# Performance work log

Hardware: AMD Instinct MI355X
Metric: run time of the kernel (lower is better)

The kernel has to match this reference:

```python
import jax, jax.numpy as jnp
import numpy as np

B, C, H, W = 32, 128, 56, 56
O = 256
KH, KW = 3, 3
SH, SW = 1, 1
PH, PW = 1, 1
T = 6          # num_terms
R = 8          # low_rank
D = C * KH * KW          # 1152
R2 = R * KH * KW         # 72


def setup_inputs() -> dict:
    key = jax.random.key(0)
    ks = jax.random.split(key, 6)
    scale = 0.05
    return {
        "x": jax.random.normal(ks[0], (B, C, H, W), dtype=jnp.float32),
        "S1s": jax.random.normal(ks[1], (T, D, R), dtype=jnp.float32) * scale,
        "U1s": jax.random.normal(ks[2], (T, R, O), dtype=jnp.float32) * scale,
        "U2s": jax.random.normal(ks[3], (T, R2, D), dtype=jnp.float32) * scale,
        "S2s": jax.random.normal(ks[4], (T, R2, O), dtype=jnp.float32) * scale,
        "bias": jax.random.normal(ks[5], (O,), dtype=jnp.float32) * scale,
    }


def _extract_windows(x):
    # im2col: pad then gather strided windows; d flattened in (C, kh, kw) order
    xp = jnp.pad(x, ((0, 0), (0, 0), (PH, PH), (PW, PW)))
    Hp, Wp = xp.shape[2], xp.shape[3]
    Ho = (Hp - KH) // SH + 1
    Wo = (Wp - KW) // SW + 1
    # stack KH*KW shifted views -> [B, C, KH*KW, Ho, Wo]
    patches = jnp.stack(
        [xp[:, :, i:i + SH * Ho:SH, j:j + SW * Wo:SW]
         for i in range(KH) for j in range(KW)],
        axis=2,
    )
    # -> [B, Ho, Wo, C, KH*KW] -> [N, C*KH*KW]
    xw = patches.transpose(0, 3, 4, 1, 2).reshape(B * Ho * Wo, D)
    return xw, Ho, Wo


def reference(x, S1s, U1s, U2s, S2s, bias):
    xw, Ho, Wo = _extract_windows(x)                    # [N, D]
    # term 1: x_windows @ S1s[t] @ U1s[t], averaged over terms
    out1 = jnp.einsum('nd,tdr,tro->no', xw, S1s, U1s, optimize=True) / T + bias
    # term 2: x_windows @ U2s[t].T @ S2s[t], averaged over terms
    out2 = jnp.einsum('nd,tdr,tro->no', xw, jnp.swapaxes(U2s, 1, 2), S2s,
                      optimize=True) / T
    # NOTE: bias is added twice, faithfully matching the original module
    out = (out1 + out2 + bias).reshape(B, Ho, Wo, O).transpose(0, 3, 1, 2)
    return out
```

## Files before the change

kernel.cpp:

```cpp
#include <hip/hip_runtime.h>
#include <hip/hip_bf16.h>

typedef __attribute__((ext_vector_type(8))) short  short8;
typedef __attribute__((ext_vector_type(8))) unsigned short ushort8;
typedef __attribute__((ext_vector_type(4))) unsigned short usv4;
typedef __attribute__((ext_vector_type(4))) float  f32x4;

#define D_DIM 1152
#define O_DIM 256
#define N_TOT 100352
#define XT_H 58
#define XT_ROW (58 * 128)

__device__ __forceinline__ unsigned short f2bf(float f) {
  __hip_bfloat16 h = __float2bfloat16(f);
  return __builtin_bit_cast(unsigned short, h);
}

#define GLOAD_LDS16(g, l)                                              \
  __builtin_amdgcn_global_load_lds(                                    \
      (const __attribute__((address_space(1))) void*)(g),              \
      (__attribute__((address_space(3))) void*)(l), 16, 0, 0)

__global__ __launch_bounds__(256) void wt_kernel(
    const float* __restrict__ S1s, const float* __restrict__ U1s,
    const float* __restrict__ U2s, const float* __restrict__ S2s,
    unsigned short* __restrict__ Wt) {
  __shared__ float A_lds[32][64];
  __shared__ float B_lds[32][64];

  const int bo = blockIdx.x & 3;
  const int bd = blockIdx.x >> 2;
  const int o0  = bo << 6;
  const int dn0 = bd << 6;
  const int rr  = dn0 >> 7;
  const int c0  = dn0 & 127;

  const int tid = threadIdx.x;
  const int ty = tid >> 4, tx = tid & 15;

  float acc[4][4] = {};

  for (int kc = 0; kc < 15; ++kc) {
#pragma unroll
    for (int e = 0; e < 8; ++e) {
      const int li = e * 256 + tid;
      const int kk = li >> 6;
      const int xx = li & 63;
      const int k  = kc * 32 + kk;
      float av, bv;
      if (k < 48) {
        av = U1s[k * O_DIM + o0 + xx];
        const int d_old = (c0 + xx) * 9 + rr;
        bv = S1s[(size_t)((k >> 3) * D_DIM + d_old) * 8 + (k & 7)];
      } else {
        const int kq = k - 48;
        av = S2s[(size_t)kq * O_DIM + o0 + xx];
        const int d_old = (c0 + xx) * 9 + rr;
        bv = U2s[(size_t)kq * D_DIM + d_old];
      }
      A_lds[kk][xx] = av;
      B_lds[kk][xx] = bv;
    }
    __syncthreads();
#pragma unroll
    for (int kk = 0; kk < 32; ++kk) {
      f32x4 a = *(const f32x4*)&A_lds[kk][ty << 2];
      f32x4 b = *(const f32x4*)&B_lds[kk][tx << 2];
#pragma unroll
      for (int i = 0; i < 4; ++i)
#pragma unroll
        for (int j = 0; j < 4; ++j)
          acc[i][j] += a[i] * b[j];
    }
    __syncthreads();
  }

#pragma unroll
  for (int i = 0; i < 4; ++i) {
    usv4 v;
#pragma unroll
    for (int j = 0; j < 4; ++j) v[j] = f2bf(acc[i][j] * (1.0f / 6.0f));
    *(usv4*)(Wt + (size_t)(o0 + (ty << 2) + i) * D_DIM + dn0 + (tx << 2)) = v;
  }
}

__global__ __launch_bounds__(256) void pad_kernel(const float* __restrict__ x,
                                                  unsigned short* __restrict__ xt) {
  int blk = blockIdx.x;
  int b = blk / XT_H, ih = blk - b * XT_H;
  unsigned short* dst = xt + (size_t)blk * XT_ROW;
  int tid = threadIdx.x;

  if (ih == 0 || ih == XT_H - 1) {
    ushort8 z;
#pragma unroll
    for (int q = 0; q < 8; ++q) z[q] = 0;
    for (int i = tid; i < XT_ROW / 8; i += 256) ((ushort8*)dst)[i] = z;
    return;
  }

  __shared__ unsigned short lds[128 * 58];
  int h = ih - 1;
  const float* xb = x + (size_t)b * 128 * 3136 + (size_t)h * 56;
#pragma unroll 4
  for (int r = 0; r < 28; ++r) {
    int idx = r * 256 + tid;
    int c = idx / 56, w2 = idx - c * 56;
    lds[c * 58 + w2] = f2bf(xb[(size_t)c * 3136 + w2]);
  }
  __syncthreads();
#pragma unroll 4
  for (int r = 0; r < 29; ++r) {
    int idx = r * 256 + tid;
    int iw = idx >> 7, c = idx & 127;
    unsigned short v = 0;
    if (iw >= 1 && iw <= 56) v = lds[c * 58 + (iw - 1)];
    dst[idx] = v;
  }
}

__device__ __forceinline__ constexpr int KOF(int kt) {
  int rr = kt >> 1;
  return ((rr / 3) * 58 + (rr % 3)) * 128 + (kt & 1) * 64;
}

#define STAGE_S(s_) do {                                                       \
  GLOAD_LDS16(pA0 + (s_) * 32, smem + ((s_) & 3) * 16384 + (tid << 3));        \
  GLOAD_LDS16(pA1 + (s_) * 32, smem + ((s_) & 3) * 16384 + 4096 + (tid << 3)); \
  GLOAD_LDS16(pB0 + KOF((s_) >> 1) + ((s_) & 1) * 32,                          \
              smem + ((s_) & 3) * 16384 + 8192 + (tid << 3));                  \
  GLOAD_LDS16(pB1 + KOF((s_) >> 1) + ((s_) & 1) * 32,                          \
              smem + ((s_) & 3) * 16384 + 12288 + (tid << 3));                 \
} while (0)

#define AFRAG(q_, row_)                                                        \
  (*(const short8*)((const char*)smem + (q_) * 32768 + (row_) * 64 +          \
      ((((lane >> 4) ^ (((row_) >> 1) & 3)) << 4))))
#define BFRAG(q_, row_)                                                        \
  (*(const short8*)((const char*)smem + (q_) * 32768 + 16384 + (row_) * 64 +  \
      ((((lane >> 4) ^ (((row_) >> 1) & 3)) << 4))))

__global__ __launch_bounds__(512, 1) void gemm_kernel(
    const unsigned short* __restrict__ Wt, const unsigned short* __restrict__ xt,
    const float* __restrict__ bias, float* __restrict__ out) {
  __shared__ __align__(1024) unsigned short smem[65536];

  const int bid   = blockIdx.x;
  const int ntile = (bid & 7) * 49 + (bid >> 3);
  const int n0    = ntile << 8;

  const int tid  = threadIdx.x;
  const int lane = tid & 63;
  const int w    = tid >> 6;
  const int wm   = w >> 2;
  const int wn   = w & 3;
  const int la15 = lane & 15;

  const int srow = tid >> 2;
  const int glog = (tid & 3) ^ ((tid >> 3) & 3);
  const unsigned short* pA0 = Wt + (size_t)srow * D_DIM + glog * 8;
  const unsigned short* pA1 = Wt + (size_t)(128 + srow) * D_DIM + glog * 8;
  const unsigned short *pB0, *pB1;
  {
    int n_g = n0 + srow;
    int b = n_g / 3136, s = n_g - b * 3136;
    int oh = s / 56, ow = s - oh * 56;
    pB0 = xt + (((size_t)b * XT_H + oh) * XT_H + ow) * 128 + glog * 8;
    n_g = n0 + 128 + srow;
    b = n_g / 3136; s = n_g - b * 3136;
    oh = s / 56; ow = s - oh * 56;
    pB1 = xt + (((size_t)b * XT_H + oh) * XT_H + ow) * 128 + glog * 8;
  }

  f32x4 acc[8][4] = {};

  STAGE_S(0);
  STAGE_S(1);
  STAGE_S(2);
  asm volatile("s_waitcnt vmcnt(8)" ::: "memory");
  __builtin_amdgcn_s_barrier();

#pragma unroll
  for (int s = 0; s < 36; ++s) {
    const int q = s & 3;

    short8 afr[8], bfr[4];
#pragma unroll
    for (int mi = 0; mi < 8; ++mi)
      afr[mi] = AFRAG(q, (wm << 7) + (mi << 4) + la15);
#pragma unroll
    for (int ni = 0; ni < 4; ++ni)
      bfr[ni] = BFRAG(q, (wn << 6) + (ni << 4) + la15);

    if (s + 3 < 36) STAGE_S(s + 3);

    if (s <= 32)      asm volatile("s_waitcnt vmcnt(8) lgkmcnt(0)" ::: "memory");
    else if (s == 33) asm volatile("s_waitcnt vmcnt(4) lgkmcnt(0)" ::: "memory");
    else              asm volatile("s_waitcnt vmcnt(0) lgkmcnt(0)" ::: "memory");
    if (s < 35) __builtin_amdgcn_s_barrier();
    __builtin_amdgcn_sched_barrier(0);

    __builtin_amdgcn_s_setprio(1);
#pragma unroll
    for (int mi = 0; mi < 8; ++mi)
#pragma unroll
      for (int ni = 0; ni < 4; ++ni)
        acc[mi][ni] = __builtin_amdgcn_mfma_f32_16x16x32_bf16(
            afr[mi], bfr[ni], acc[mi][ni], 0, 0, 0);
    __builtin_amdgcn_s_setprio(0);
  }

  const int lr = (lane >> 4) << 2;
#pragma unroll
  for (int ni = 0; ni < 4; ++ni) {
    const int ng = n0 + (wn << 6) + (ni << 4) + la15;
    const int b  = ng / 3136;
    const int s  = ng - b * 3136;
    float* op = out + (size_t)b * (O_DIM * 3136) + s;
#pragma unroll
    for (int mi = 0; mi < 8; ++mi) {
      const int og = (wm << 7) + (mi << 4) + lr;
#pragma unroll
      for (int r = 0; r < 4; ++r)
        op[(size_t)(og + r) * 3136] = acc[mi][ni][r] + 2.0f * bias[og + r];
    }
  }
}

extern "C" void kernel_launch(void* const* d_in, const int* in_sizes, int n_in,
                              void* d_out, int out_size, void* d_ws, size_t ws_size,
                              hipStream_t stream) {
  const float* x    = (const float*)d_in[0];
  const float* S1s  = (const float*)d_in[1];
  const float* U1s  = (const float*)d_in[2];
  const float* U2s  = (const float*)d_in[3];
  const float* S2s  = (const float*)d_in[4];
  const float* bias = (const float*)d_in[5];
  float* out = (float*)d_out;
  (void)ws_size;

  unsigned short* xt = (unsigned short*)d_ws;
  unsigned short* Wt = (unsigned short*)((char*)d_ws + (size_t)32 * XT_H * XT_ROW * 2);

  pad_kernel<<<dim3(32 * XT_H), dim3(256), 0, stream>>>(x, xt);
  wt_kernel<<<dim3(72), dim3(256), 0, stream>>>(S1s, U1s, U2s, S2s, Wt);
  gemm_kernel<<<dim3(392), dim3(512), 0, stream>>>(Wt, xt, bias, out);
}
```

Baseline: 122.2 us.

## Shrink GEMM tile to 256x128 with 3-stage LDS ring for two blocks per CU

```diff
diff --git a/kernel.cpp b/kernel.cpp
--- a/kernel.cpp
+++ b/kernel.cpp
@@ -120,86 +120,80 @@
   }
 }
 
-__device__ __forceinline__ constexpr int KOF(int kt) {
-  int rr = kt >> 1;
-  return ((rr / 3) * 58 + (rr % 3)) * 128 + (kt & 1) * 64;
+__device__ __forceinline__ constexpr int KOFS(int s) {
+  int rr = s >> 2;
+  return ((rr / 3) * 58 + (rr % 3)) * 128 + (s & 3) * 32;
 }
 
 #define STAGE_S(s_) do {                                                       \
-  GLOAD_LDS16(pA0 + (s_) * 32, smem + ((s_) & 3) * 16384 + (tid << 3));        \
-  GLOAD_LDS16(pA1 + (s_) * 32, smem + ((s_) & 3) * 16384 + 4096 + (tid << 3)); \
-  GLOAD_LDS16(pB0 + KOF((s_) >> 1) + ((s_) & 1) * 32,                          \
-              smem + ((s_) & 3) * 16384 + 8192 + (tid << 3));                  \
-  GLOAD_LDS16(pB1 + KOF((s_) >> 1) + ((s_) & 1) * 32,                          \
-              smem + ((s_) & 3) * 16384 + 12288 + (tid << 3));                 \
+  const int _sl = ((s_) % 3) * 12288;                                          \
+  GLOAD_LDS16(pA[0] + (s_) * 32, smem + _sl + (tid << 3));                     \
+  GLOAD_LDS16(pA[1] + (s_) * 32, smem + _sl + 2048 + (tid << 3));              \
+  GLOAD_LDS16(pA[2] + (s_) * 32, smem + _sl + 4096 + (tid << 3));              \
+  GLOAD_LDS16(pA[3] + (s_) * 32, smem + _sl + 6144 + (tid << 3));              \
+  GLOAD_LDS16(pB[0] + KOFS(s_), smem + _sl + 8192 + (tid << 3));               \
+  GLOAD_LDS16(pB[1] + KOFS(s_), smem + _sl + 10240 + (tid << 3));              \
 } while (0)
 
-#define AFRAG(q_, row_)                                                        \
-  (*(const short8*)((const char*)smem + (q_) * 32768 + (row_) * 64 +          \
-      ((((lane >> 4) ^ (((row_) >> 1) & 3)) << 4))))
-#define BFRAG(q_, row_)                                                        \
-  (*(const short8*)((const char*)smem + (q_) * 32768 + 16384 + (row_) * 64 +  \
-      ((((lane >> 4) ^ (((row_) >> 1) & 3)) << 4))))
-
-__global__ __launch_bounds__(512, 1) void gemm_kernel(
+#define AFRAG(sl_, row_)                                                       \
+  (*(const short8*)((const char*)smem + (sl_) * 24576 + (row_) * 64 +        \
+      (((lane >> 4) ^ (((row_) >> 1) & 3)) << 4)))
+#define BFRAG(sl_, row_)                                                       \
+  (*(const short8*)((const char*)smem + (sl_) * 24576 + 16384 + (row_) * 64 + \
+      (((lane >> 4) ^ (((row_) >> 1) & 3)) << 4)))
+
+__global__ __launch_bounds__(256, 2) void gemm_kernel(
     const unsigned short* __restrict__ Wt, const unsigned short* __restrict__ xt,
     const float* __restrict__ bias, float* __restrict__ out) {
-  __shared__ __align__(1024) unsigned short smem[65536];
+  __shared__ __align__(1024) unsigned short smem[36864];
 
   const int bid   = blockIdx.x;
-  const int ntile = (bid & 7) * 49 + (bid >> 3);
-  const int n0    = ntile << 8;
+  const int ntile = (bid & 7) * 98 + (bid >> 3);
+  const int n0    = ntile << 7;
 
   const int tid  = threadIdx.x;
   const int lane = tid & 63;
   const int w    = tid >> 6;
-  const int wm   = w >> 2;
-  const int wn   = w & 3;
+  const int wm   = w >> 1;
+  const int wn   = w & 1;
   const int la15 = lane & 15;
 
   const int srow = tid >> 2;
-  const int glog = (tid & 3) ^ ((tid >> 3) & 3);
-  const unsigned short* pA0 = Wt + (size_t)srow * D_DIM + glog * 8;
-  const unsigned short* pA1 = Wt + (size_t)(128 + srow) * D_DIM + glog * 8;
-  const unsigned short *pB0, *pB1;
-  {
-    int n_g = n0 + srow;
-    int b = n_g / 3136, s = n_g - b * 3136;
-    int oh = s / 56, ow = s - oh * 56;
-    pB0 = xt + (((size_t)b * XT_H + oh) * XT_H + ow) * 128 + glog * 8;
-    n_g = n0 + 128 + srow;
-    b = n_g / 3136; s = n_g - b * 3136;
-    oh = s / 56; ow = s - oh * 56;
-    pB1 = xt + (((size_t)b * XT_H + oh) * XT_H + ow) * 128 + glog * 8;
+  const int sg   = (tid & 3) ^ ((tid >> 3) & 3);
+  const unsigned short* pA[4];
+  const unsigned short* pB[2];
+#pragma unroll
+  for (int r = 0; r < 4; ++r)
+    pA[r] = Wt + (size_t)(r * 64 + srow) * D_DIM + sg * 8;
+#pragma unroll
+  for (int r = 0; r < 2; ++r) {
+    const int n_g = n0 + r * 64 + srow;
+    const int b   = n_g / 3136;
+    const int s   = n_g - b * 3136;
+    const int oh  = s / 56, ow = s - oh * 56;
+    pB[r] = xt + (((size_t)b * XT_H + oh) * XT_H + ow) * 128 + sg * 8;
   }
 
   f32x4 acc[8][4] = {};
 
   STAGE_S(0);
   STAGE_S(1);
-  STAGE_S(2);
-  asm volatile("s_waitcnt vmcnt(8)" ::: "memory");
+  asm volatile("s_waitcnt vmcnt(6)" ::: "memory");
   __builtin_amdgcn_s_barrier();
 
 #pragma unroll
   for (int s = 0; s < 36; ++s) {
-    const int q = s & 3;
+    const int sl = s % 3;
 
     short8 afr[8], bfr[4];
 #pragma unroll
     for (int mi = 0; mi < 8; ++mi)
-      afr[mi] = AFRAG(q, (wm << 7) + (mi << 4) + la15);
+      afr[mi] = AFRAG(sl, (wm << 7) + (mi << 4) + la15);
 #pragma unroll
     for (int ni = 0; ni < 4; ++ni)
-      bfr[ni] = BFRAG(q, (wn << 6) + (ni << 4) + la15);
-
-    if (s + 3 < 36) STAGE_S(s + 3);
-
-    if (s <= 32)      asm volatile("s_waitcnt vmcnt(8) lgkmcnt(0)" ::: "memory");
-    else if (s == 33) asm volatile("s_waitcnt vmcnt(4) lgkmcnt(0)" ::: "memory");
-    else              asm volatile("s_waitcnt vmcnt(0) lgkmcnt(0)" ::: "memory");
-    if (s < 35) __builtin_amdgcn_s_barrier();
-    __builtin_amdgcn_sched_barrier(0);
+      bfr[ni] = BFRAG(sl, (wn << 6) + (ni << 4) + la15);
+
+    if (s + 2 < 36) STAGE_S(s + 2);
 
     __builtin_amdgcn_s_setprio(1);
 #pragma unroll
@@ -209,6 +203,10 @@
         acc[mi][ni] = __builtin_amdgcn_mfma_f32_16x16x32_bf16(
             afr[mi], bfr[ni], acc[mi][ni], 0, 0, 0);
     __builtin_amdgcn_s_setprio(0);
+
+    if (s < 34)       asm volatile("s_waitcnt vmcnt(6)" ::: "memory");
+    else if (s == 34) asm volatile("s_waitcnt vmcnt(0)" ::: "memory");
+    if (s < 35) __builtin_amdgcn_s_barrier();
   }
 
   const int lr = (lane >> 4) << 2;
@@ -245,5 +243,5 @@
 
   pad_kernel<<<dim3(32 * XT_H), dim3(256), 0, stream>>>(x, xt);
   wt_kernel<<<dim3(72), dim3(256), 0, stream>>>(S1s, U1s, U2s, S2s, Wt);
-  gemm_kernel<<<dim3(392), dim3(512), 0, stream>>>(Wt, xt, bias, out);
-}
+  gemm_kernel<<<dim3(784), dim3(256), 0, stream>>>(Wt, xt, bias, out);
+}
```

After: 127.6 us. +4.4%, slower.
